# Optimization experiments

Measured on AMD Instinct MI355X. Metric: run time of the kernel, lower is better.

## Reference

```python
import jax, jax.numpy as jnp
import numpy as np

FP16_MIN = -65504.0  # torch.finfo(torch.float16).min


def addcoords(x):
    # x: (b, c, h, w) NCHW. AddCoords(rank=1, with_r=True): appends a
    # y-coordinate channel (normalized over h, broadcast over w) and |y-0.5|.
    b, c, h, w = x.shape
    yy = (jnp.arange(h, dtype=x.dtype) / (h - 1)) * 2.0 - 1.0  # (h,)
    yy = jnp.broadcast_to(yy[None, None, :, None], (b, 1, h, w))
    rr = jnp.abs(yy - 0.5)
    return jnp.concatenate([x, yy, rr], axis=1)


def conv1x1(x, W, b):
    # W: (c_out, c_in), b: (c_out,)
    return jnp.einsum('bihw,oi->bohw', x, W) + b[None, :, None, None]


def setup_inputs() -> dict:
    key = jax.random.key(0)
    ks = jax.random.split(key, 16)
    c = 64
    B2, h, w = 4, 256, 256
    s_in = 0.02
    inp = {
        'x': jax.random.normal(ks[0], (B2, c, h, w), jnp.float32),
        'res_enc': jax.random.normal(ks[1], (B2, c, h, w), jnp.float32),
        'tr_feat': jax.random.normal(ks[2], (B2, c, h, w), jnp.float32),
        # CoordConv 1x1 weights take c+2 input channels (coord + r channels)
        'Wl1': jax.random.normal(ks[3], (c, c + 2), jnp.float32) * s_in,
        'bl1': jax.random.normal(ks[4], (c,), jnp.float32) * s_in,
        'Wr1': jax.random.normal(ks[5], (c, c + 2), jnp.float32) * s_in,
        'br1': jax.random.normal(ks[6], (c,), jnp.float32) * s_in,
        'Wl2': jax.random.normal(ks[7], (c, c), jnp.float32) * s_in,
        'bl2': jax.random.normal(ks[8], (c,), jnp.float32) * s_in,
        'Wr2': jax.random.normal(ks[9], (c, c), jnp.float32) * s_in,
        'br2': jax.random.normal(ks[10], (c,), jnp.float32) * s_in,
        'beta1': jax.random.normal(ks[11], (1, c, 1, 1), jnp.float32) * s_in,
        'gamma1': jax.random.normal(ks[12], (1, c, 1, 1), jnp.float32) * s_in,
        'beta3': jax.random.normal(ks[13], (1, c, 1, 1), jnp.float32) * s_in,
        'gamma3': jax.random.normal(ks[14], (1, c, 1, 1), jnp.float32) * s_in,
    }
    return inp


def reference(x, res_enc, tr_feat, Wl1, bl1, Wr1, br1, Wl2, bl2, Wr2, br2,
              beta1, gamma1, beta3, gamma3):
    x_l, x_r = jnp.split(x, 2, axis=0)
    re_l, re_r = jnp.split(res_enc, 2, axis=0)
    tr_l, tr_r = jnp.split(tr_feat, 2, axis=0)
    b, c, h, w = x_l.shape
    scale = jnp.asarray(c, x.dtype) ** -0.5

    Q = conv1x1(addcoords(x_l), Wl1, bl1) + beta1 * tr_l   # (b, c, h, w)
    S = conv1x1(addcoords(x_r), Wr1, br1) + beta1 * tr_r   # (b, c, h, w)

    # per-row (epipolar) attention along width: score[b,h,i,j]
    score = jnp.einsum('bchi,bchj->bhij', Q, S) * scale
    idx = jnp.arange(w)
    upper = idx[None, :] > idx[:, None]  # strict upper triangle (j > i)
    score = jnp.where(upper[None, None], FP16_MIN, score)
    # In torch, score_T is a view of score; after in-place masking, score_T
    # masked at strict-lower positions == transpose of masked score.
    M_r2l = jax.nn.softmax(score, axis=-1)                       # (b,h,w,w)
    M_l2r = jax.nn.softmax(jnp.swapaxes(score, -1, -2), axis=-1)  # (b,h,w,w)

    buf_R = conv1x1(x_r, Wr2, br2) + gamma1 * re_r  # (b, c, h, w)
    buf_l = jnp.einsum('bhij,bchj->bchi', M_r2l, buf_R)
    buf_L = conv1x1(x_l, Wl2, bl2) + gamma1 * re_l
    buf_r = jnp.einsum('bhij,bchj->bchi', M_l2r, buf_L)

    out_L = x_l + beta3 * buf_l
    out_R = x_r + gamma3 * buf_r
    return jnp.concatenate([out_L, out_R], axis=0)
```

## Files before the change

kernel.cpp:

```cpp
#include <hip/hip_runtime.h>
#include <stdint.h>

#define HW 65536
#define C_ 64

typedef __attribute__((ext_vector_type(8))) short short8;
typedef __attribute__((ext_vector_type(4))) float f32x4;
typedef long long i64;

#define MFMA16(a, b, c) __builtin_amdgcn_mfma_f32_16x16x32_bf16((a), (b), (c), 0, 0, 0)
#define MFMA8(a, b, c)  __builtin_amdgcn_mfma_f32_16x16x32_fp8_fp8((a), (b), (c), 0, 0, 0)

union U16x8 { uint4 q; short8 v; uint32_t u[4]; };
union PU { uint32_t u[2]; i64 q; };

__device__ inline uint32_t pack_bf16(float lo, float hi) {
  uint32_t ul = __float_as_uint(lo), uh = __float_as_uint(hi);
  ul = (ul + 0x7fffu + ((ul >> 16) & 1u)) >> 16;
  uh = (uh + 0x7fffu + ((uh >> 16) & 1u)) >> 16;
  return ul | (uh << 16);
}
__device__ inline short8 ld8bf(const uint16_t* p) {
  U16x8 t; t.q = *(const uint4*)p; return t.v;
}
__device__ inline i64 ld8f8(const uint8_t* p) { return *(const i64*)p; }
__device__ inline uint32_t pk4f8(float a, float b, float c, float d) {
  uint32_t v = __builtin_amdgcn_cvt_pk_fp8_f32(a, b, 0, false);
  v = __builtin_amdgcn_cvt_pk_fp8_f32(c, d, v, true);
  return v;
}

__device__ inline int qf_idx(int p, int c) { return p * 64 + (c ^ ((p & 7) << 3)); }
__device__ inline int vf_idx(int c, int j) { return c * 256 + (j ^ ((c & 7) << 3)); }
__device__ inline int wf_idx(int r, int k) { return r * 64 + (k ^ ((r & 7) << 3)); }

__global__ __launch_bounds__(512, 2) void SCAM_73151882985874_kernel(
    const float* __restrict__ x, const float* __restrict__ res_enc,
    const float* __restrict__ tr_feat,
    const float* __restrict__ Wl1, const float* __restrict__ bl1,
    const float* __restrict__ Wr1, const float* __restrict__ br1,
    const float* __restrict__ Wl2, const float* __restrict__ bl2,
    const float* __restrict__ Wr2, const float* __restrict__ br2,
    const float* __restrict__ beta1, const float* __restrict__ gamma1,
    const float* __restrict__ beta3, const float* __restrict__ gamma3,
    float* __restrict__ out)
{
  __shared__ __align__(16) uint8_t sQ[16384];
  __shared__ __align__(16) uint8_t sS[16384];
  __shared__ __align__(16) uint8_t sVL[16384];
  __shared__ __align__(16) uint8_t sVR[16384];
  __shared__ __align__(16) uint16_t sW[16384];

  const int tid = threadIdx.x;
  const int wid = tid >> 6, lane = tid & 63, g = lane >> 4, li = lane & 15;
  const int bb = blockIdx.x >> 8, hh = blockIdx.x & 255;
  const float yy = (float)hh * (2.0f / 255.0f) - 1.0f;
  const float rr = fabsf(yy - 0.5f);

  const size_t rowoff = (size_t)hh * 256;
  const float* xl  = x + ((size_t)bb * C_) * HW + rowoff;
  const float* xr  = x + ((size_t)(2 + bb) * C_) * HW + rowoff;
  const float* trl = tr_feat + ((size_t)bb * C_) * HW + rowoff;
  const float* trr = tr_feat + ((size_t)(2 + bb) * C_) * HW + rowoff;
  const float* rel = res_enc + ((size_t)bb * C_) * HW + rowoff;
  const float* rer = res_enc + ((size_t)(2 + bb) * C_) * HW + rowoff;
  float* outL = out + ((size_t)bb * C_) * HW + rowoff;
  float* outR = out + ((size_t)(2 + bb) * C_) * HW + rowoff;

  {
    const int r = tid >> 3, k0 = (tid & 7) * 8;
    const float* Ws[4] = {Wl1, Wr1, Wl2, Wr2};
    const int ldws[4] = {66, 66, 64, 64};
    #pragma unroll
    for (int m = 0; m < 4; ++m) {
      const float* src = Ws[m] + (size_t)r * ldws[m] + k0;
      U16x8 t8;
      t8.u[0] = pack_bf16(src[0], src[1]); t8.u[1] = pack_bf16(src[2], src[3]);
      t8.u[2] = pack_bf16(src[4], src[5]); t8.u[3] = pack_bf16(src[6], src[7]);
      *(uint4*)&sW[m * 4096 + wf_idx(r, k0)] = t8.q;
    }
  }

  auto ldXside = [&](const float* __restrict__ src, short8 bx[2][2]) {
    float xv[2][2][8];
    #pragma unroll
    for (int ptl = 0; ptl < 2; ++ptl) {
      int pix = wid * 32 + ptl * 16 + li;
      #pragma unroll
      for (int kk = 0; kk < 2; ++kk) {
        const float* s = src + (size_t)(kk * 32 + g * 8) * HW + pix;
        #pragma unroll
        for (int j = 0; j < 8; ++j) xv[ptl][kk][j] = s[(size_t)j * HW];
      }
    }
    #pragma unroll
    for (int ptl = 0; ptl < 2; ++ptl)
      #pragma unroll
      for (int kk = 0; kk < 2; ++kk) {
        U16x8 t8;
        t8.u[0] = pack_bf16(xv[ptl][kk][0], xv[ptl][kk][1]);
        t8.u[1] = pack_bf16(xv[ptl][kk][2], xv[ptl][kk][3]);
        t8.u[2] = pack_bf16(xv[ptl][kk][4], xv[ptl][kk][5]);
        t8.u[3] = pack_bf16(xv[ptl][kk][6], xv[ptl][kk][7]);
        bx[ptl][kk] = t8.v;
      }
  };

  auto conv_one = [&](int widx, const float* __restrict__ Wc,
                      const float* __restrict__ bias, const float* __restrict__ mod,
                      const float* __restrict__ E,
                      const short8 bx[2][2], uint8_t* dstQS, uint8_t* dstV) {
    float ev[2][4][4];
    #pragma unroll
    for (int ptl = 0; ptl < 2; ++ptl) {
      int pix = wid * 32 + ptl * 16 + li;
      #pragma unroll
      for (int ct = 0; ct < 4; ++ct)
        #pragma unroll
        for (int r = 0; r < 4; ++r)
          ev[ptl][ct][r] = E[(size_t)(ct * 16 + 4 * g + r) * HW + pix];
    }
    float be[4][4], md[4][4];
    #pragma unroll
    for (int ct = 0; ct < 4; ++ct)
      #pragma unroll
      for (int r = 0; r < 4; ++r) {
        int c = ct * 16 + 4 * g + r;
        float b = bias[c];
        if (Wc) b += Wc[(size_t)c * 66 + 64] * yy + Wc[(size_t)c * 66 + 65] * rr;
        be[ct][r] = b;
        md[ct][r] = mod[c];
      }
    const uint16_t* wb = sW + widx * 4096;
    #pragma unroll
    for (int ct = 0; ct < 4; ++ct) {
      short8 af0 = ld8bf(&wb[wf_idx(ct * 16 + li, g * 8)]);
      short8 af1 = ld8bf(&wb[wf_idx(ct * 16 + li, 32 + g * 8)]);
      #pragma unroll
      for (int ptl = 0; ptl < 2; ++ptl) {
        int pix = wid * 32 + ptl * 16 + li;
        f32x4 acc = {0.f, 0.f, 0.f, 0.f};
        acc = MFMA16(af0, bx[ptl][0], acc);
        acc = MFMA16(af1, bx[ptl][1], acc);
        float v[4];
        #pragma unroll
        for (int r = 0; r < 4; ++r) v[r] = acc[r] + be[ct][r] + md[ct][r] * ev[ptl][ct][r];
        if (dstV) {
          uint32_t pk = pk4f8(v[0], v[1], v[2], v[3]);
          #pragma unroll
          for (int r = 0; r < 4; ++r)
            dstV[vf_idx(ct * 16 + 4 * g + r, pix)] = (uint8_t)(pk >> (8 * r));
        } else {
          *(uint32_t*)&dstQS[qf_idx(pix, ct * 16 + 4 * g)] = pk4f8(v[0], v[1], v[2], v[3]);
        }
      }
    }
  };

  {
    short8 bx[2][2];
    ldXside(xl, bx);
    __syncthreads();
    conv_one(0, Wl1, bl1, beta1,  trl, bx, sQ, nullptr);
    conv_one(2, nullptr, bl2, gamma1, rel, bx, nullptr, sVL);
  }
  {
    short8 bx[2][2];
    ldXside(xr, bx);
    conv_one(1, Wr1, br1, beta1,  trr, bx, sS, nullptr);
    conv_one(3, nullptr, br2, gamma1, rer, bx, nullptr, sVR);
  }
  __syncthreads();

  const int addr_lo = ((((g & 1) << 1) << 4) + li) << 2;
  const int addr_hi = addr_lo + 64;
  const bool hiD = (g >= 2);
  const int j0 = wid * 32;

  {
    i64 bS00 = ld8f8(&sS[qf_idx(j0 + li, g * 8)]);
    i64 bS01 = ld8f8(&sS[qf_idx(j0 + li, 32 + g * 8)]);
    i64 bS10 = ld8f8(&sS[qf_idx(j0 + 16 + li, g * 8)]);
    i64 bS11 = ld8f8(&sS[qf_idx(j0 + 16 + li, 32 + g * 8)]);
    f32x4 acc[4][2];
    #pragma unroll
    for (int ct = 0; ct < 4; ++ct) { acc[ct][0] = (f32x4){0,0,0,0}; acc[ct][1] = (f32x4){0,0,0,0}; }
    float zp0 = 0.f, zp1 = 0.f;

    for (int ip = wid; ip < 8; ++ip) {
      i64 aQ00 = ld8f8(&sQ[qf_idx(ip * 32 + li, g * 8)]);
      i64 aQ01 = ld8f8(&sQ[qf_idx(ip * 32 + li, 32 + g * 8)]);
      i64 aQ10 = ld8f8(&sQ[qf_idx(ip * 32 + 16 + li, g * 8)]);
      i64 aQ11 = ld8f8(&sQ[qf_idx(ip * 32 + 16 + li, 32 + g * 8)]);
      i64 aV0 = ld8f8(&sVL[vf_idx(li,      ip * 32 + g * 8)]);
      i64 aV1 = ld8f8(&sVL[vf_idx(16 + li, ip * 32 + g * 8)]);
      i64 aV2 = ld8f8(&sVL[vf_idx(32 + li, ip * 32 + g * 8)]);
      i64 aV3 = ld8f8(&sVL[vf_idx(48 + li, ip * 32 + g * 8)]);
      const int a0 = ip * 32 + 4 * g;
      #pragma unroll
      for (int jt = 0; jt < 2; ++jt) {
        const int jj = j0 + jt * 16 + li;
        const i64 b0 = jt ? bS10 : bS00;
        const i64 b1 = jt ? bS11 : bS01;
        f32x4 s0 = {0.f, 0.f, 0.f, 0.f};
        s0 = MFMA8(aQ00, b0, s0); s0 = MFMA8(aQ01, b1, s0);
        f32x4 s1 = {0.f, 0.f, 0.f, 0.f};
        s1 = MFMA8(aQ10, b0, s1); s1 = MFMA8(aQ11, b1, s1);
        float ps = 0.f, p0[4], p1[4];
        #pragma unroll
        for (int r = 0; r < 4; ++r) {
          p0[r] = (a0 + r >= jj)      ? __expf(s0[r] * 0.125f) : 0.f;
          p1[r] = (a0 + 16 + r >= jj) ? __expf(s1[r] * 0.125f) : 0.f;
          ps += p0[r] + p1[r];
        }
        if (jt == 0) zp0 += ps; else zp1 += ps;
        uint32_t D0 = pk4f8(p0[0], p0[1], p0[2], p0[3]);
        uint32_t D1 = pk4f8(p1[0], p1[1], p1[2], p1[3]);
        int w00 = __builtin_amdgcn_ds_bpermute(addr_lo, (int)D0);
        int w01 = __builtin_amdgcn_ds_bpermute(addr_lo, (int)D1);
        int w10 = __builtin_amdgcn_ds_bpermute(addr_hi, (int)D0);
        int w11 = __builtin_amdgcn_ds_bpermute(addr_hi, (int)D1);
        PU t;
        t.u[0] = hiD ? (uint32_t)w01 : (uint32_t)w00;
        t.u[1] = hiD ? (uint32_t)w11 : (uint32_t)w10;
        const i64 bP = t.q;
        acc[0][jt] = MFMA8(aV0, bP, acc[0][jt]);
        acc[1][jt] = MFMA8(aV1, bP, acc[1][jt]);
        acc[2][jt] = MFMA8(aV2, bP, acc[2][jt]);
        acc[3][jt] = MFMA8(aV3, bP, acc[3][jt]);
      }
    }
    float res[2][4][4];
    #pragma unroll
    for (int jt = 0; jt < 2; ++jt) {
      int j = j0 + jt * 16 + li;
      #pragma unroll
      for (int ct = 0; ct < 4; ++ct)
        #pragma unroll
        for (int r = 0; r < 4; ++r)
          res[jt][ct][r] = xr[(size_t)(ct * 16 + 4 * g + r) * HW + j];
    }
    zp0 += __shfl_xor(zp0, 16); zp0 += __shfl_xor(zp0, 32);
    zp1 += __shfl_xor(zp1, 16); zp1 += __shfl_xor(zp1, 32);
    #pragma unroll
    for (int jt = 0; jt < 2; ++jt) {
      float invz = 1.0f / (jt == 0 ? zp0 : zp1);
      int j = j0 + jt * 16 + li;
      #pragma unroll
      for (int ct = 0; ct < 4; ++ct)
        #pragma unroll
        for (int r = 0; r < 4; ++r) {
          int c = ct * 16 + 4 * g + r;
          outR[(size_t)c * HW + j] =
              fmaf(gamma3[c], acc[ct][jt][r] * invz, res[jt][ct][r]);
        }
    }
  }

  {
    i64 bQ00 = ld8f8(&sQ[qf_idx(j0 + li, g * 8)]);
    i64 bQ01 = ld8f8(&sQ[qf_idx(j0 + li, 32 + g * 8)]);
    i64 bQ10 = ld8f8(&sQ[qf_idx(j0 + 16 + li, g * 8)]);
    i64 bQ11 = ld8f8(&sQ[qf_idx(j0 + 16 + li, 32 + g * 8)]);
    f32x4 acc[4][2];
    #pragma unroll
    for (int ct = 0; ct < 4; ++ct) { acc[ct][0] = (f32x4){0,0,0,0}; acc[ct][1] = (f32x4){0,0,0,0}; }
    float zp0 = 0.f, zp1 = 0.f;

    for (int jp = 0; jp <= wid; ++jp) {
      i64 aS00 = ld8f8(&sS[qf_idx(jp * 32 + li, g * 8)]);
      i64 aS01 = ld8f8(&sS[qf_idx(jp * 32 + li, 32 + g * 8)]);
      i64 aS10 = ld8f8(&sS[qf_idx(jp * 32 + 16 + li, g * 8)]);
      i64 aS11 = ld8f8(&sS[qf_idx(jp * 32 + 16 + li, 32 + g * 8)]);
      i64 aV0 = ld8f8(&sVR[vf_idx(li,      jp * 32 + g * 8)]);
      i64 aV1 = ld8f8(&sVR[vf_idx(16 + li, jp * 32 + g * 8)]);
      i64 aV2 = ld8f8(&sVR[vf_idx(32 + li, jp * 32 + g * 8)]);
      i64 aV3 = ld8f8(&sVR[vf_idx(48 + li, jp * 32 + g * 8)]);
      const int a0 = jp * 32 + 4 * g;
      #pragma unroll
      for (int itl = 0; itl < 2; ++itl) {
        const int ii = j0 + itl * 16 + li;
        const i64 b0 = itl ? bQ10 : bQ00;
        const i64 b1 = itl ? bQ11 : bQ01;
        f32x4 s0 = {0.f, 0.f, 0.f, 0.f};
        s0 = MFMA8(aS00, b0, s0); s0 = MFMA8(aS01, b1, s0);
        f32x4 s1 = {0.f, 0.f, 0.f, 0.f};
        s1 = MFMA8(aS10, b0, s1); s1 = MFMA8(aS11, b1, s1);
        float ps = 0.f, p0[4], p1[4];
        #pragma unroll
        for (int r = 0; r < 4; ++r) {
          p0[r] = (a0 + r <= ii)      ? __expf(s0[r] * 0.125f) : 0.f;
          p1[r] = (a0 + 16 + r <= ii) ? __expf(s1[r] * 0.125f) : 0.f;
          ps += p0[r] + p1[r];
        }
        if (itl == 0) zp0 += ps; else zp1 += ps;
        uint32_t D0 = pk4f8(p0[0], p0[1], p0[2], p0[3]);
        uint32_t D1 = pk4f8(p1[0], p1[1], p1[2], p1[3]);
        int w00 = __builtin_amdgcn_ds_bpermute(addr_lo, (int)D0);
        int w01 = __builtin_amdgcn_ds_bpermute(addr_lo, (int)D1);
        int w10 = __builtin_amdgcn_ds_bpermute(addr_hi, (int)D0);
        int w11 = __builtin_amdgcn_ds_bpermute(addr_hi, (int)D1);
        PU t;
        t.u[0] = hiD ? (uint32_t)w01 : (uint32_t)w00;
        t.u[1] = hiD ? (uint32_t)w11 : (uint32_t)w10;
        const i64 bP = t.q;
        acc[0][itl] = MFMA8(aV0, bP, acc[0][itl]);
        acc[1][itl] = MFMA8(aV1, bP, acc[1][itl]);
        acc[2][itl] = MFMA8(aV2, bP, acc[2][itl]);
        acc[3][itl] = MFMA8(aV3, bP, acc[3][itl]);
      }
    }
    float res[2][4][4];
    #pragma unroll
    for (int itl = 0; itl < 2; ++itl) {
      int i = j0 + itl * 16 + li;
      #pragma unroll
      for (int ct = 0; ct < 4; ++ct)
        #pragma unroll
        for (int r = 0; r < 4; ++r)
          res[itl][ct][r] = xl[(size_t)(ct * 16 + 4 * g + r) * HW + i];
    }
    zp0 += __shfl_xor(zp0, 16); zp0 += __shfl_xor(zp0, 32);
    zp1 += __shfl_xor(zp1, 16); zp1 += __shfl_xor(zp1, 32);
    #pragma unroll
    for (int itl = 0; itl < 2; ++itl) {
      float invz = 1.0f / (itl == 0 ? zp0 : zp1);
      int i = j0 + itl * 16 + li;
      #pragma unroll
      for (int ct = 0; ct < 4; ++ct)
        #pragma unroll
        for (int r = 0; r < 4; ++r) {
          int c = ct * 16 + 4 * g + r;
          outL[(size_t)c * HW + i] =
              fmaf(beta3[c], acc[ct][itl][r] * invz, res[itl][ct][r]);
        }
    }
  }
}

extern "C" void kernel_launch(void* const* d_in, const int* in_sizes, int n_in,
                              void* d_out, int out_size, void* d_ws, size_t ws_size,
                              hipStream_t stream) {
  const float* x       = (const float*)d_in[0];
  const float* res_enc = (const float*)d_in[1];
  const float* tr_feat = (const float*)d_in[2];
  const float* Wl1     = (const float*)d_in[3];
  const float* bl1     = (const float*)d_in[4];
  const float* Wr1     = (const float*)d_in[5];
  const float* br1     = (const float*)d_in[6];
  const float* Wl2     = (const float*)d_in[7];
  const float* bl2     = (const float*)d_in[8];
  const float* Wr2     = (const float*)d_in[9];
  const float* br2     = (const float*)d_in[10];
  const float* beta1   = (const float*)d_in[11];
  const float* gamma1  = (const float*)d_in[12];
  const float* beta3   = (const float*)d_in[13];
  const float* gamma3  = (const float*)d_in[14];
  float* outp = (float*)d_out;

  dim3 grid(512);
  dim3 block(512);
  SCAM_73151882985874_kernel<<<grid, block, 0, stream>>>(
      x, res_enc, tr_feat, Wl1, bl1, Wr1, br1, Wl2, bl2, Wr2, br2,
      beta1, gamma1, beta3, gamma3, outp);
}
```

Measured before the change: 75.01 us.

## Split fused kernel into conv and attention kernels via global workspace

```diff
diff --git a/kernel.cpp b/kernel.cpp
--- a/kernel.cpp
+++ b/kernel.cpp
@@ -34,7 +34,7 @@
 __device__ inline int vf_idx(int c, int j) { return c * 256 + (j ^ ((c & 7) << 3)); }
 __device__ inline int wf_idx(int r, int k) { return r * 64 + (k ^ ((r & 7) << 3)); }
 
-__global__ __launch_bounds__(512, 2) void SCAM_73151882985874_kernel(
+__global__ __launch_bounds__(512, 4) void SCAM_conv(
     const float* __restrict__ x, const float* __restrict__ res_enc,
     const float* __restrict__ tr_feat,
     const float* __restrict__ Wl1, const float* __restrict__ bl1,
@@ -42,18 +42,14 @@
     const float* __restrict__ Wl2, const float* __restrict__ bl2,
     const float* __restrict__ Wr2, const float* __restrict__ br2,
     const float* __restrict__ beta1, const float* __restrict__ gamma1,
-    const float* __restrict__ beta3, const float* __restrict__ gamma3,
-    float* __restrict__ out)
+    uint8_t* __restrict__ ws, int row0)
 {
-  __shared__ __align__(16) uint8_t sQ[16384];
-  __shared__ __align__(16) uint8_t sS[16384];
-  __shared__ __align__(16) uint8_t sVL[16384];
-  __shared__ __align__(16) uint8_t sVR[16384];
   __shared__ __align__(16) uint16_t sW[16384];
 
   const int tid = threadIdx.x;
   const int wid = tid >> 6, lane = tid & 63, g = lane >> 4, li = lane & 15;
-  const int bb = blockIdx.x >> 8, hh = blockIdx.x & 255;
+  const int rp = row0 + blockIdx.x;
+  const int bb = rp >> 8, hh = rp & 255;
   const float yy = (float)hh * (2.0f / 255.0f) - 1.0f;
   const float rr = fabsf(yy - 0.5f);
 
@@ -64,8 +60,7 @@
   const float* trr = tr_feat + ((size_t)(2 + bb) * C_) * HW + rowoff;
   const float* rel = res_enc + ((size_t)bb * C_) * HW + rowoff;
   const float* rer = res_enc + ((size_t)(2 + bb) * C_) * HW + rowoff;
-  float* outL = out + ((size_t)bb * C_) * HW + rowoff;
-  float* outR = out + ((size_t)(2 + bb) * C_) * HW + rowoff;
+  uint8_t* base = ws + (size_t)blockIdx.x * 65536;
 
   {
     const int r = tid >> 3, k0 = (tid & 7) * 8;
@@ -106,10 +101,10 @@
       }
   };
 
-  auto conv_one = [&](int widx, const float* __restrict__ Wc,
-                      const float* __restrict__ bias, const float* __restrict__ mod,
-                      const float* __restrict__ E,
-                      const short8 bx[2][2], uint8_t* dstQS, uint8_t* dstV) {
+  auto conv_g = [&](int widx, const float* __restrict__ Wc,
+                    const float* __restrict__ bias, const float* __restrict__ mod,
+                    const float* __restrict__ E,
+                    const short8 bx[2][2], uint8_t* dstQS, uint8_t* dstV) {
     float ev[2][4][4];
     #pragma unroll
     for (int ptl = 0; ptl < 2; ++ptl) {
@@ -145,13 +140,13 @@
         float v[4];
         #pragma unroll
         for (int r = 0; r < 4; ++r) v[r] = acc[r] + be[ct][r] + md[ct][r] * ev[ptl][ct][r];
+        uint32_t pk = pk4f8(v[0], v[1], v[2], v[3]);
         if (dstV) {
-          uint32_t pk = pk4f8(v[0], v[1], v[2], v[3]);
           #pragma unroll
           for (int r = 0; r < 4; ++r)
-            dstV[vf_idx(ct * 16 + 4 * g + r, pix)] = (uint8_t)(pk >> (8 * r));
+            dstV[(size_t)(ct * 16 + 4 * g + r) * 256 + pix] = (uint8_t)(pk >> (8 * r));
         } else {
-          *(uint32_t*)&dstQS[qf_idx(pix, ct * 16 + 4 * g)] = pk4f8(v[0], v[1], v[2], v[3]);
+          *(uint32_t*)&dstQS[pix * 64 + ct * 16 + 4 * g] = pk;
         }
       }
     }
@@ -161,27 +156,60 @@
     short8 bx[2][2];
     ldXside(xl, bx);
     __syncthreads();
-    conv_one(0, Wl1, bl1, beta1,  trl, bx, sQ, nullptr);
-    conv_one(2, nullptr, bl2, gamma1, rel, bx, nullptr, sVL);
+    conv_g(0, Wl1, bl1, beta1,  trl, bx, base, nullptr);
+    conv_g(2, nullptr, bl2, gamma1, rel, bx, nullptr, base + 32768);
   }
   {
     short8 bx[2][2];
     ldXside(xr, bx);
-    conv_one(1, Wr1, br1, beta1,  trr, bx, sS, nullptr);
-    conv_one(3, nullptr, br2, gamma1, rer, bx, nullptr, sVR);
+    conv_g(1, Wr1, br1, beta1,  trr, bx, base + 16384, nullptr);
+    conv_g(3, nullptr, br2, gamma1, rer, bx, nullptr, base + 49152);
+  }
+}
+
+__global__ __launch_bounds__(512, 4) void SCAM_attn(
+    const float* __restrict__ x,
+    const float* __restrict__ beta3, const float* __restrict__ gamma3,
+    const uint8_t* __restrict__ ws, float* __restrict__ out, int row0)
+{
+  __shared__ __align__(16) uint8_t sQ[16384];
+  __shared__ __align__(16) uint8_t sS[16384];
+  __shared__ __align__(16) uint8_t sVL[16384];
+  __shared__ __align__(16) uint8_t sVR[16384];
+
+  const int tid = threadIdx.x;
+  const int wid = tid >> 6, lane = tid & 63, g = lane >> 4, li = lane & 15;
+  const int rp = row0 + blockIdx.x;
+  const int bb = rp >> 8, hh = rp & 255;
+  const size_t rowoff = (size_t)hh * 256;
+  const float* xl = x + ((size_t)bb * C_) * HW + rowoff;
+  const float* xr = x + ((size_t)(2 + bb) * C_) * HW + rowoff;
+  float* outL = out + ((size_t)bb * C_) * HW + rowoff;
+  float* outR = out + ((size_t)(2 + bb) * C_) * HW + rowoff;
+  const uint8_t* base = ws + (size_t)blockIdx.x * 65536;
+
+  for (int t = tid; t < 2048; t += 512) {
+    int pix = t >> 3, c0 = (t & 7) * 8;
+    int sw = (pix & 7) << 3;
+    *(uint2*)&sQ[pix * 64 + (c0 ^ sw)] = *(const uint2*)&base[pix * 64 + c0];
+    *(uint2*)&sS[pix * 64 + (c0 ^ sw)] = *(const uint2*)&base[16384 + pix * 64 + c0];
+    int c = t >> 5, j0 = (t & 31) * 8;
+    int swv = (c & 7) << 3;
+    *(uint2*)&sVL[c * 256 + (j0 ^ swv)] = *(const uint2*)&base[32768 + c * 256 + j0];
+    *(uint2*)&sVR[c * 256 + (j0 ^ swv)] = *(const uint2*)&base[49152 + c * 256 + j0];
   }
   __syncthreads();
 
   const int addr_lo = ((((g & 1) << 1) << 4) + li) << 2;
   const int addr_hi = addr_lo + 64;
   const bool hiD = (g >= 2);
-  const int j0 = wid * 32;
+  const int j0w = wid * 32;
 
   {
-    i64 bS00 = ld8f8(&sS[qf_idx(j0 + li, g * 8)]);
-    i64 bS01 = ld8f8(&sS[qf_idx(j0 + li, 32 + g * 8)]);
-    i64 bS10 = ld8f8(&sS[qf_idx(j0 + 16 + li, g * 8)]);
-    i64 bS11 = ld8f8(&sS[qf_idx(j0 + 16 + li, 32 + g * 8)]);
+    i64 bS00 = ld8f8(&sS[qf_idx(j0w + li, g * 8)]);
+    i64 bS01 = ld8f8(&sS[qf_idx(j0w + li, 32 + g * 8)]);
+    i64 bS10 = ld8f8(&sS[qf_idx(j0w + 16 + li, g * 8)]);
+    i64 bS11 = ld8f8(&sS[qf_idx(j0w + 16 + li, 32 + g * 8)]);
     f32x4 acc[4][2];
     #pragma unroll
     for (int ct = 0; ct < 4; ++ct) { acc[ct][0] = (f32x4){0,0,0,0}; acc[ct][1] = (f32x4){0,0,0,0}; }
@@ -199,7 +227,7 @@
       const int a0 = ip * 32 + 4 * g;
       #pragma unroll
       for (int jt = 0; jt < 2; ++jt) {
-        const int jj = j0 + jt * 16 + li;
+        const int jj = j0w + jt * 16 + li;
         const i64 b0 = jt ? bS10 : bS00;
         const i64 b1 = jt ? bS11 : bS01;
         f32x4 s0 = {0.f, 0.f, 0.f, 0.f};
@@ -233,7 +261,7 @@
     float res[2][4][4];
     #pragma unroll
     for (int jt = 0; jt < 2; ++jt) {
-      int j = j0 + jt * 16 + li;
+      int j = j0w + jt * 16 + li;
       #pragma unroll
       for (int ct = 0; ct < 4; ++ct)
         #pragma unroll
@@ -245,7 +273,7 @@
     #pragma unroll
     for (int jt = 0; jt < 2; ++jt) {
       float invz = 1.0f / (jt == 0 ? zp0 : zp1);
-      int j = j0 + jt * 16 + li;
+      int j = j0w + jt * 16 + li;
       #pragma unroll
       for (int ct = 0; ct < 4; ++ct)
         #pragma unroll
@@ -258,10 +286,10 @@
   }
 
   {
-    i64 bQ00 = ld8f8(&sQ[qf_idx(j0 + li, g * 8)]);
-    i64 bQ01 = ld8f8(&sQ[qf_idx(j0 + li, 32 + g * 8)]);
-    i64 bQ10 = ld8f8(&sQ[qf_idx(j0 + 16 + li, g * 8)]);
-    i64 bQ11 = ld8f8(&sQ[qf_idx(j0 + 16 + li, 32 + g * 8)]);
+    i64 bQ00 = ld8f8(&sQ[qf_idx(j0w + li, g * 8)]);
+    i64 bQ01 = ld8f8(&sQ[qf_idx(j0w + li, 32 + g * 8)]);
+    i64 bQ10 = ld8f8(&sQ[qf_idx(j0w + 16 + li, g * 8)]);
+    i64 bQ11 = ld8f8(&sQ[qf_idx(j0w + 16 + li, 32 + g * 8)]);
     f32x4 acc[4][2];
     #pragma unroll
     for (int ct = 0; ct < 4; ++ct) { acc[ct][0] = (f32x4){0,0,0,0}; acc[ct][1] = (f32x4){0,0,0,0}; }
@@ -279,7 +307,7 @@
       const int a0 = jp * 32 + 4 * g;
       #pragma unroll
       for (int itl = 0; itl < 2; ++itl) {
-        const int ii = j0 + itl * 16 + li;
+        const int ii = j0w + itl * 16 + li;
         const i64 b0 = itl ? bQ10 : bQ00;
         const i64 b1 = itl ? bQ11 : bQ01;
         f32x4 s0 = {0.f, 0.f, 0.f, 0.f};
@@ -313,7 +341,7 @@
     float res[2][4][4];
     #pragma unroll
     for (int itl = 0; itl < 2; ++itl) {
-      int i = j0 + itl * 16 + li;
+      int i = j0w + itl * 16 + li;
       #pragma unroll
       for (int ct = 0; ct < 4; ++ct)
         #pragma unroll
@@ -325,7 +353,7 @@
     #pragma unroll
     for (int itl = 0; itl < 2; ++itl) {
       float invz = 1.0f / (itl == 0 ? zp0 : zp1);
-      int i = j0 + itl * 16 + li;
+      int i = j0w + itl * 16 + li;
       #pragma unroll
       for (int ct = 0; ct < 4; ++ct)
         #pragma unroll
@@ -357,10 +385,19 @@
   const float* beta3   = (const float*)d_in[13];
   const float* gamma3  = (const float*)d_in[14];
   float* outp = (float*)d_out;
-
-  dim3 grid(512);
-  dim3 block(512);
-  SCAM_73151882985874_kernel<<<grid, block, 0, stream>>>(
-      x, res_enc, tr_feat, Wl1, bl1, Wr1, br1, Wl2, bl2, Wr2, br2,
-      beta1, gamma1, beta3, gamma3, outp);
-}
+  uint8_t* ws = (uint8_t*)d_ws;
+
+  int rows_per_chunk = (int)(ws_size / 65536);
+  if (rows_per_chunk > 512) rows_per_chunk = 512;
+  if (rows_per_chunk < 1) rows_per_chunk = 1;
+
+  for (int row0 = 0; row0 < 512; row0 += rows_per_chunk) {
+    int n = 512 - row0;
+    if (n > rows_per_chunk) n = rows_per_chunk;
+    SCAM_conv<<<dim3(n), dim3(512), 0, stream>>>(
+        x, res_enc, tr_feat, Wl1, bl1, Wr1, br1, Wl2, bl2, Wr2, br2,
+        beta1, gamma1, ws, row0);
+    SCAM_attn<<<dim3(n), dim3(512), 0, stream>>>(
+        x, beta3, gamma3, ws, outp, row0);
+  }
+}
```

Result: slower. 180.5 us (+140.7%).
